# Optimization experiments

Hardware: AMD Instinct MI355X
Metric: run time of the kernel (lower is better)

## Reference

```python
import jax, jax.numpy as jnp
import numpy as np

DIM = 1024
HEADS = 16
MLP = 4096
EPS = 1e-5

def _layer_norm(x, g, b):
    mu = jnp.mean(x, axis=-1, keepdims=True)
    var = jnp.mean(jnp.square(x - mu), axis=-1, keepdims=True)
    return (x - mu) * jax.lax.rsqrt(var + EPS) * g + b

def setup_inputs() -> dict:
    key = jax.random.key(0)
    ks = jax.random.split(key, 8)
    s = 0.02
    return {
        "x": jax.random.normal(ks[0], (2, 2048, DIM), dtype=jnp.float32),
        "ln1_g": jnp.ones((DIM,), jnp.float32),
        "ln1_b": jnp.zeros((DIM,), jnp.float32),
        "qkv_w": jax.random.normal(ks[1], (DIM, 3 * DIM), jnp.float32) * s,
        "qkv_b": jnp.zeros((3 * DIM,), jnp.float32),
        "proj_w": jax.random.normal(ks[2], (DIM, DIM), jnp.float32) * s,
        "proj_b": jnp.zeros((DIM,), jnp.float32),
        "ln2_g": jnp.ones((DIM,), jnp.float32),
        "ln2_b": jnp.zeros((DIM,), jnp.float32),
        "fc1_w": jax.random.normal(ks[3], (DIM, MLP), jnp.float32) * s,
        "fc1_b": jnp.zeros((MLP,), jnp.float32),
        "fc2_w": jax.random.normal(ks[4], (MLP, DIM), jnp.float32) * s,
        "fc2_b": jnp.zeros((DIM,), jnp.float32),
    }

def reference(x, ln1_g, ln1_b, qkv_w, qkv_b, proj_w, proj_b,
              ln2_g, ln2_b, fc1_w, fc1_b, fc2_w, fc2_b):
    B, N, C = x.shape
    H = HEADS
    D = C // H
    # --- attention (pre-norm); NOTE: source applies no 1/sqrt(D) scaling ---
    h = _layer_norm(x, ln1_g, ln1_b)
    qkv = (h @ qkv_w + qkv_b).reshape(B, N, 3, H, D)
    q, k, v = (qkv[:, :, 0], qkv[:, :, 1], qkv[:, :, 2])  # [B,N,H,D]
    qk = jnp.einsum('bnhd,bmhd->bhnm', q, k)
    attn = jax.nn.softmax(qk, axis=-1)
    y = jnp.einsum('bhnm,bmhd->bnhd', attn, v).reshape(B, N, C)
    y = y @ proj_w + proj_b
    x = x + y
    # --- MLP (pre-norm), exact GELU like torch nn.GELU ---
    h2 = _layer_norm(x, ln2_g, ln2_b)
    h2 = jax.nn.gelu(h2 @ fc1_w + fc1_b, approximate=False)
    x = x + (h2 @ fc2_w + fc2_b)
    return x
```

## Files before the change

### kernel.cpp

```cpp
#include <hip/hip_runtime.h>
#include <hip/hip_bf16.h>

#define CDIM   1024
#define NSEQ   2048
#define NHEAD  16
#define HDIM   64
#define MLPDIM 4096
#define TROWS  4096

typedef __attribute__((ext_vector_type(8)))  __bf16 bf16x8;
typedef __attribute__((ext_vector_type(4)))  float  f32x4;
typedef __attribute__((ext_vector_type(16))) float  f32x16;
typedef __attribute__((ext_vector_type(4)))  unsigned short us4;

static __device__ __forceinline__ unsigned short f2bf(float f) {
  unsigned int u = __float_as_uint(f);
  u += 0x7fffu + ((u >> 16) & 1u);
  return (unsigned short)(u >> 16);
}

#define MFMA16(a, b, c) __builtin_amdgcn_mfma_f32_16x16x32_bf16(a, b, c, 0, 0, 0)
#define MFMA32(a, b, c) __builtin_amdgcn_mfma_f32_32x32x16_bf16(a, b, c, 0, 0, 0)

static __device__ __forceinline__ void gll16(const unsigned short* g, unsigned short* l) {
  __builtin_amdgcn_global_load_lds(
      (const __attribute__((address_space(1))) unsigned int*)g,
      (__attribute__((address_space(3))) unsigned int*)l, 16, 0, 0);
}

__global__ __launch_bounds__(256)
void ln_bf16_kernel(const float* __restrict__ x,
                    const float* __restrict__ gam,
                    const float* __restrict__ bet,
                    unsigned short* __restrict__ out)
{
  int row = blockIdx.x;
  int t = threadIdx.x;
  const float4* xr = (const float4*)(x + (size_t)row * CDIM);
  float4 v = xr[t];
  float s  = v.x + v.y + v.z + v.w;
  float s2 = v.x*v.x + v.y*v.y + v.z*v.z + v.w*v.w;
  #pragma unroll
  for (int off = 32; off > 0; off >>= 1) {
    s  += __shfl_down(s, off);
    s2 += __shfl_down(s2, off);
  }
  __shared__ float rs[4], rs2[4];
  int wave = t >> 6, lane = t & 63;
  if (lane == 0) { rs[wave] = s; rs2[wave] = s2; }
  __syncthreads();
  float fs  = rs[0] + rs[1] + rs[2] + rs[3];
  float fs2 = rs2[0] + rs2[1] + rs2[2] + rs2[3];
  float mu   = fs * (1.0f / CDIM);
  float var  = fs2 * (1.0f / CDIM) - mu * mu;
  float rstd = rsqrtf(var + 1e-5f);
  float4 gg = ((const float4*)gam)[t];
  float4 bb = ((const float4*)bet)[t];
  us4 o;
  o.x = f2bf((v.x - mu) * rstd * gg.x + bb.x);
  o.y = f2bf((v.y - mu) * rstd * gg.y + bb.y);
  o.z = f2bf((v.z - mu) * rstd * gg.z + bb.z);
  o.w = f2bf((v.w - mu) * rstd * gg.w + bb.w);
  ((us4*)(out + (size_t)row * CDIM))[t] = o;
}

__global__ __launch_bounds__(256)
void wt_bf16_kernel(const float* __restrict__ W, unsigned short* __restrict__ Wt,
                    int K, int N)
{
  __shared__ float tile[32][33];
  int n0 = blockIdx.x * 32, k0 = blockIdx.y * 32;
  int t = threadIdx.x;
  int r = t >> 3, c4 = (t & 7) << 2;
  float4 v = *(const float4*)(W + (size_t)(k0 + r) * N + n0 + c4);
  tile[r][c4 + 0] = v.x; tile[r][c4 + 1] = v.y;
  tile[r][c4 + 2] = v.z; tile[r][c4 + 3] = v.w;
  __syncthreads();
  us4 o;
  o.x = f2bf(tile[c4 + 0][r]);
  o.y = f2bf(tile[c4 + 1][r]);
  o.z = f2bf(tile[c4 + 2][r]);
  o.w = f2bf(tile[c4 + 3][r]);
  *(us4*)(Wt + (size_t)(n0 + r) * K + k0 + c4) = o;
}

template<int EPI>
__global__ __launch_bounds__(256, 4)
void gemm_bt(const unsigned short* __restrict__ A, const unsigned short* __restrict__ Bt,
             const float* __restrict__ bias, int Kstride, int Kc, int nbx, int nby,
             float* __restrict__ outf, unsigned short* __restrict__ outb,
             const float* __restrict__ resid, float* __restrict__ pp,
             unsigned short* __restrict__ qo, unsigned short* __restrict__ ko,
             unsigned short* __restrict__ vo)
{
  __shared__ unsigned short As[2][128 * 32];
  __shared__ unsigned short Bs[2][128 * 32];
  const int tid  = threadIdx.x;
  const int lane = tid & 63;
  const int wave = tid >> 6;
  const int wr = wave >> 1, wc = wave & 1;
  const int g = lane >> 4, r16 = lane & 15;

  const int nwg = gridDim.x;
  const int orig = ((int)blockIdx.x & 7) * (nwg >> 3) + ((int)blockIdx.x >> 3);
  const int bx = orig % nbx;
  const int t2 = orig / nbx;
  const int by = t2 % nby;
  const int kz = t2 / nby;
  const int bm = by * 128, bn = bx * 128;
  const int kbase = kz * Kc;
  const int N = nbx * 128;

  auto stage = [&](int d, int k0) {
    #pragma unroll
    for (int c = 0; c < 2; c++) {
      int o   = (c * 256 + tid) << 3;
      int row = o >> 5;
      int col = o & 31;
      int ub  = (c * 256 + (tid & ~63)) << 3;
      gll16(A  + (size_t)(bm + row) * Kstride + kbase + k0 + col, &As[d][ub]);
      gll16(Bt + (size_t)(bn + row) * Kstride + kbase + k0 + col, &Bs[d][ub]);
    }
  };

  f32x4 acc[4][4];
  #pragma unroll
  for (int i = 0; i < 4; i++)
    #pragma unroll
    for (int j = 0; j < 4; j++) acc[i][j] = (f32x4){0.f, 0.f, 0.f, 0.f};

  stage(0, 0);
  const int nkt = Kc / 32;
  for (int kt = 0; kt < nkt; kt++) {
    const int cur = kt & 1;
    __syncthreads();
    if (kt + 1 < nkt) stage(cur ^ 1, (kt + 1) * 32);
    bf16x8 af[4], bfr[4];
    #pragma unroll
    for (int i = 0; i < 4; i++) {
      int row = wr * 64 + i * 16 + r16;
      af[i] = *(const bf16x8*)(&As[cur][row * 32 + 8 * g]);
    }
    #pragma unroll
    for (int j = 0; j < 4; j++) {
      int row = wc * 64 + j * 16 + r16;
      bfr[j] = *(const bf16x8*)(&Bs[cur][row * 32 + 8 * g]);
    }
    __builtin_amdgcn_s_setprio(1);
    #pragma unroll
    for (int i = 0; i < 4; i++)
      #pragma unroll
      for (int j = 0; j < 4; j++)
        acc[i][j] = MFMA16(af[i], bfr[j], acc[i][j]);
    __builtin_amdgcn_s_setprio(0);
  }

  #pragma unroll
  for (int i = 0; i < 4; i++) {
    #pragma unroll
    for (int j = 0; j < 4; j++) {
      int col = bn + wc * 64 + j * 16 + r16;
      float bv = (EPI == 2 && kz != 0) ? 0.f : bias[col];
      #pragma unroll
      for (int jj = 0; jj < 4; jj++) {
        int row = bm + wr * 64 + i * 16 + 4 * g + jj;
        float val = acc[i][j][jj] + bv;
        if (EPI == 1) {
          int sel = col >> 10, cc = col & 1023;
          int hh = cc >> 6, d = cc & 63;
          int b = row >> 11, tk = row & 2047;
          size_t hb = (size_t)(b * NHEAD + hh);
          if (sel == 0)      qo[(hb * NSEQ + tk) * HDIM + d] = f2bf(val * 1.4426950408889634f);
          else if (sel == 1) ko[(hb * NSEQ + tk) * HDIM + d] = f2bf(val);
          else               vo[(hb * HDIM + d) * NSEQ + tk] = f2bf(val);
        } else if (EPI == 2) {
          size_t idx = (size_t)row * N + col;
          if (kz == 0) outf[idx] = val + resid[idx];
          else         pp[idx]   = val;
        } else {
          float ge = 0.5f * val * (1.0f + erff(val * 0.70710678118654752f));
          outb[(size_t)row * N + col] = f2bf(ge);
        }
      }
    }
  }
}

__global__ __launch_bounds__(256)
void add_kernel(float* __restrict__ out, const float* __restrict__ pp, int n4)
{
  int i = blockIdx.x * 256 + threadIdx.x;
  int stride = gridDim.x * 256;
  for (; i < n4; i += stride) {
    float4 a = ((const float4*)out)[i];
    float4 b = ((const float4*)pp)[i];
    a.x += b.x; a.y += b.y; a.z += b.z; a.w += b.w;
    ((float4*)out)[i] = a;
  }
}

__global__ __launch_bounds__(256, 2)
void attn_kernel(const unsigned short* __restrict__ q, const unsigned short* __restrict__ k,
                 const unsigned short* __restrict__ vt, unsigned short* __restrict__ y)
{
  int bid = blockIdx.x;
  int xcd = bid & 7, loc = bid >> 3;
  int bh  = xcd * 4 + (loc >> 4);
  int qchunk = loc & 15;
  int b = bh >> 4, h = bh & 15;
  int wave = threadIdx.x >> 6, lane = threadIdx.x & 63;
  int ql = lane & 31;
  int hi = lane >> 5;
  int q0 = qchunk * 128 + wave * 32;
  const unsigned short* qb = q  + (size_t)bh * NSEQ * HDIM;
  const unsigned short* kb = k  + (size_t)bh * NSEQ * HDIM;
  const unsigned short* vb = vt + (size_t)bh * HDIM * NSEQ;

  __shared__ unsigned short KL[2][2048];
  __shared__ unsigned short VL[2][2048];

  auto stage = [&](int d, int it) {
    int kv0 = it * 32;
    {
      int c = wave * 64 + lane;
      int row = c >> 3, col = c & 7;
      int sc  = (row << 3) | (col ^ (row & 7));
      gll16(kb + (size_t)kv0 * HDIM + sc * 8, &KL[d][wave * 512]);
    }
    {
      int c = wave * 64 + lane;
      int row = c >> 2, col = c & 3;
      int scol = col ^ ((row >> 1) & 3);
      gll16(vb + (size_t)row * NSEQ + kv0 + scol * 8, &VL[d][wave * 512]);
    }
  };

  bf16x8 aq[4];
  #pragma unroll
  for (int s = 0; s < 4; s++)
    aq[s] = *(const bf16x8*)(qb + (size_t)(q0 + ql) * HDIM + s * 16 + hi * 8);

  float ssum = 0.f;
  f32x16 o0, o1;
  #pragma unroll
  for (int r = 0; r < 16; r++) { o0[r] = 0.f; o1[r] = 0.f; }

  stage(0, 0);
  for (int it = 0; it < NSEQ / 32; it++) {
    const int cur = it & 1;
    __syncthreads();
    if (it + 1 < NSEQ / 32) stage(cur ^ 1, it + 1);
    bf16x8 kf[4];
    #pragma unroll
    for (int s = 0; s < 4; s++)
      kf[s] = *(const bf16x8*)((const char*)KL[cur] +
               ql * 128 + ((((s << 1) | hi) ^ (ql & 7)) << 4));
    f32x16 sacc;
    #pragma unroll
    for (int r = 0; r < 16; r++) sacc[r] = -32.0f;
    __builtin_amdgcn_s_setprio(1);
    #pragma unroll
    for (int s = 0; s < 4; s++)
      sacc = MFMA32(kf[s], aq[s], sacc);
    __builtin_amdgcn_s_setprio(0);
    float ps = 0.f;
    #pragma unroll
    for (int r = 0; r < 16; r++) {
      sacc[r] = exp2f(sacc[r]);
      ps += sacc[r];
    }
    ssum += ps;
    bf16x8 vf[2][2];
    #pragma unroll
    for (int t = 0; t < 2; t++)
      #pragma unroll
      for (int db = 0; db < 2; db++)
        vf[t][db] = *(const bf16x8*)((const char*)VL[cur] +
                     (db * 32 + ql) * 64 + ((((t << 1) | hi) ^ ((ql >> 1) & 3)) << 4));
    __builtin_amdgcn_s_setprio(1);
    #pragma unroll
    for (int t = 0; t < 2; t++) {
      unsigned pk01, pk23, pk45, pk67;
      asm("v_cvt_pk_bf16_f32 %0, %1, %2" : "=v"(pk01) : "v"(sacc[8*t+0]), "v"(sacc[8*t+1]));
      asm("v_cvt_pk_bf16_f32 %0, %1, %2" : "=v"(pk23) : "v"(sacc[8*t+2]), "v"(sacc[8*t+3]));
      asm("v_cvt_pk_bf16_f32 %0, %1, %2" : "=v"(pk45) : "v"(sacc[8*t+4]), "v"(sacc[8*t+5]));
      asm("v_cvt_pk_bf16_f32 %0, %1, %2" : "=v"(pk67) : "v"(sacc[8*t+6]), "v"(sacc[8*t+7]));
      asm("v_permlane32_swap_b32 %0, %1" : "+v"(pk01), "+v"(pk45));
      asm("v_permlane32_swap_b32 %0, %1" : "+v"(pk23), "+v"(pk67));
      union { unsigned u[4]; bf16x8 v; } pf;
      pf.u[0] = pk01; pf.u[1] = pk23; pf.u[2] = pk45; pf.u[3] = pk67;
      o0 = MFMA32(vf[t][0], pf.v, o0);
      o1 = MFMA32(vf[t][1], pf.v, o1);
    }
    __builtin_amdgcn_s_setprio(0);
  }
  float stot = ssum + __shfl_xor(ssum, 32);
  float inv = 1.0f / stot;
  unsigned short* yr = y + ((size_t)(b * NSEQ + q0 + ql)) * CDIM + h * HDIM;
  #pragma unroll
  for (int db = 0; db < 2; db++) {
    const f32x16& oo = db ? o1 : o0;
    #pragma unroll
    for (int rq = 0; rq < 4; rq++) {
      us4 w;
      w.x = f2bf(oo[4*rq+0] * inv);
      w.y = f2bf(oo[4*rq+1] * inv);
      w.z = f2bf(oo[4*rq+2] * inv);
      w.w = f2bf(oo[4*rq+3] * inv);
      *(us4*)(yr + db * 32 + rq * 8 + hi * 4) = w;
    }
  }
}

extern "C" void kernel_launch(void* const* d_in, const int* in_sizes, int n_in,
                              void* d_out, int out_size, void* d_ws, size_t ws_size,
                              hipStream_t stream)
{
  const float* x      = (const float*)d_in[0];
  const float* ln1_g  = (const float*)d_in[1];
  const float* ln1_b  = (const float*)d_in[2];
  const float* qkv_w  = (const float*)d_in[3];
  const float* qkv_b  = (const float*)d_in[4];
  const float* proj_w = (const float*)d_in[5];
  const float* proj_b = (const float*)d_in[6];
  const float* ln2_g  = (const float*)d_in[7];
  const float* ln2_b  = (const float*)d_in[8];
  const float* fc1_w  = (const float*)d_in[9];
  const float* fc1_b  = (const float*)d_in[10];
  const float* fc2_w  = (const float*)d_in[11];
  const float* fc2_b  = (const float*)d_in[12];
  float* out = (float*)d_out;

  char* p = (char*)d_ws;
  size_t off = 0;
  auto alloc = [&](size_t bytes) -> void* {
    void* r = p + off; off += (bytes + 255) & ~(size_t)255; return r;
  };
  unsigned short* wt_qkv  = (unsigned short*)alloc((size_t)3072 * 1024 * 2);
  unsigned short* wt_proj = (unsigned short*)alloc((size_t)1024 * 1024 * 2);
  unsigned short* wt_fc1  = (unsigned short*)alloc((size_t)4096 * 1024 * 2);
  unsigned short* wt_fc2  = (unsigned short*)alloc((size_t)1024 * 4096 * 2);
  unsigned short* h1  = (unsigned short*)alloc((size_t)TROWS * CDIM * 2);
  unsigned short* qb  = (unsigned short*)alloc((size_t)TROWS * CDIM * 2);
  unsigned short* kb  = (unsigned short*)alloc((size_t)TROWS * CDIM * 2);
  unsigned short* vtb = (unsigned short*)alloc((size_t)TROWS * CDIM * 2);
  unsigned short* yb  = (unsigned short*)alloc((size_t)TROWS * CDIM * 2);
  float*          x1  = (float*)alloc((size_t)TROWS * CDIM * 4);
  unsigned short* h2  = (unsigned short*)alloc((size_t)TROWS * CDIM * 2);
  unsigned short* g1  = (unsigned short*)alloc((size_t)TROWS * MLPDIM * 2);
  float* pp = (float*)qb;

  dim3 blk(256);
  wt_bf16_kernel<<<dim3(3072 / 32, 1024 / 32), blk, 0, stream>>>(qkv_w, wt_qkv, 1024, 3072);
  wt_bf16_kernel<<<dim3(1024 / 32, 1024 / 32), blk, 0, stream>>>(proj_w, wt_proj, 1024, 1024);
  wt_bf16_kernel<<<dim3(4096 / 32, 1024 / 32), blk, 0, stream>>>(fc1_w, wt_fc1, 1024, 4096);
  wt_bf16_kernel<<<dim3(1024 / 32, 4096 / 32), blk, 0, stream>>>(fc2_w, wt_fc2, 4096, 1024);
  ln_bf16_kernel<<<TROWS, blk, 0, stream>>>(x, ln1_g, ln1_b, h1);
  gemm_bt<1><<<dim3(768), blk, 0, stream>>>(
      h1, wt_qkv, qkv_b, 1024, 1024, 24, 32,
      nullptr, nullptr, nullptr, nullptr, qb, kb, vtb);
  attn_kernel<<<dim3(512), blk, 0, stream>>>(qb, kb, vtb, yb);
  gemm_bt<2><<<dim3(512), blk, 0, stream>>>(
      yb, wt_proj, proj_b, 1024, 512, 8, 32,
      x1, nullptr, x, pp, nullptr, nullptr, nullptr);
  add_kernel<<<dim3(2048), blk, 0, stream>>>(x1, pp, TROWS * CDIM / 4);
  ln_bf16_kernel<<<TROWS, blk, 0, stream>>>(x1, ln2_g, ln2_b, h2);
  gemm_bt<3><<<dim3(1024), blk, 0, stream>>>(
      h2, wt_fc1, fc1_b, 1024, 1024, 32, 32,
      nullptr, g1, nullptr, nullptr, nullptr, nullptr, nullptr);
  gemm_bt<2><<<dim3(512), blk, 0, stream>>>(
      g1, wt_fc2, fc2_b, 4096, 2048, 8, 32,
      out, nullptr, x1, pp, nullptr, nullptr, nullptr);
  add_kernel<<<dim3(2048), blk, 0, stream>>>(out, pp, TROWS * CDIM / 4);
}
```

Before: 295.4 us.

## Split attention KV range across waves, fuse add into LN2, approximate GELU

The attention kernel now handles 64 query rows per block, with two wave pairs each covering half of the KV sequence. Partial outputs and sums are merged through shared memory, and the grid doubles to 1024 blocks at higher occupancy. This adds parallelism and occupancy for attention at the cost of an extra reduction step. Separately, the split-K residual add is folded into the second layernorm, removing one kernel launch and a full pass over memory. Exact erf GELU is replaced by a sigmoid-style exp2 approximation, which is cheaper but changes numerics slightly.

```diff
diff --git a/kernel.cpp b/kernel.cpp
--- a/kernel.cpp
+++ b/kernel.cpp
@@ -38,6 +38,45 @@
   int t = threadIdx.x;
   const float4* xr = (const float4*)(x + (size_t)row * CDIM);
   float4 v = xr[t];
+  float s  = v.x + v.y + v.z + v.w;
+  float s2 = v.x*v.x + v.y*v.y + v.z*v.z + v.w*v.w;
+  #pragma unroll
+  for (int off = 32; off > 0; off >>= 1) {
+    s  += __shfl_down(s, off);
+    s2 += __shfl_down(s2, off);
+  }
+  __shared__ float rs[4], rs2[4];
+  int wave = t >> 6, lane = t & 63;
+  if (lane == 0) { rs[wave] = s; rs2[wave] = s2; }
+  __syncthreads();
+  float fs  = rs[0] + rs[1] + rs[2] + rs[3];
+  float fs2 = rs2[0] + rs2[1] + rs2[2] + rs2[3];
+  float mu   = fs * (1.0f / CDIM);
+  float var  = fs2 * (1.0f / CDIM) - mu * mu;
+  float rstd = rsqrtf(var + 1e-5f);
+  float4 gg = ((const float4*)gam)[t];
+  float4 bb = ((const float4*)bet)[t];
+  us4 o;
+  o.x = f2bf((v.x - mu) * rstd * gg.x + bb.x);
+  o.y = f2bf((v.y - mu) * rstd * gg.y + bb.y);
+  o.z = f2bf((v.z - mu) * rstd * gg.z + bb.z);
+  o.w = f2bf((v.w - mu) * rstd * gg.w + bb.w);
+  ((us4*)(out + (size_t)row * CDIM))[t] = o;
+}
+
+__global__ __launch_bounds__(256)
+void ln_add_bf16_kernel(float* __restrict__ x, const float* __restrict__ pp,
+                        const float* __restrict__ gam, const float* __restrict__ bet,
+                        unsigned short* __restrict__ out)
+{
+  int row = blockIdx.x;
+  int t = threadIdx.x;
+  float4* xr = (float4*)(x + (size_t)row * CDIM);
+  const float4* pr = (const float4*)(pp + (size_t)row * CDIM);
+  float4 v = xr[t];
+  float4 q = pr[t];
+  v.x += q.x; v.y += q.y; v.z += q.z; v.w += q.w;
+  xr[t] = v;
   float s  = v.x + v.y + v.z + v.w;
   float s2 = v.x*v.x + v.y*v.y + v.z*v.z + v.w*v.w;
   #pragma unroll
@@ -178,7 +217,9 @@
           if (kz == 0) outf[idx] = val + resid[idx];
           else         pp[idx]   = val;
         } else {
-          float ge = 0.5f * val * (1.0f + erff(val * 0.70710678118654752f));
+          float vv = val * val;
+          float u2 = val * (2.3022361f + 0.1029445f * vv);
+          float ge = val - val / (1.0f + exp2f(u2));
           outb[(size_t)row * N + col] = f2bf(ge);
         }
       }
@@ -199,39 +240,43 @@
   }
 }
 
-__global__ __launch_bounds__(256, 2)
+__global__ __launch_bounds__(256, 4)
 void attn_kernel(const unsigned short* __restrict__ q, const unsigned short* __restrict__ k,
                  const unsigned short* __restrict__ vt, unsigned short* __restrict__ y)
 {
   int bid = blockIdx.x;
   int xcd = bid & 7, loc = bid >> 3;
-  int bh  = xcd * 4 + (loc >> 4);
-  int qchunk = loc & 15;
+  int bh  = xcd * 4 + (loc >> 5);
+  int qb64 = loc & 31;
   int b = bh >> 4, h = bh & 15;
   int wave = threadIdx.x >> 6, lane = threadIdx.x & 63;
+  int qt = wave >> 1, kvh = wave & 1;
   int ql = lane & 31;
   int hi = lane >> 5;
-  int q0 = qchunk * 128 + wave * 32;
+  int q0 = qb64 * 64 + qt * 32;
+  const int kvbase = kvh * (NSEQ / 2);
   const unsigned short* qb = q  + (size_t)bh * NSEQ * HDIM;
   const unsigned short* kb = k  + (size_t)bh * NSEQ * HDIM;
   const unsigned short* vb = vt + (size_t)bh * HDIM * NSEQ;
 
-  __shared__ unsigned short KL[2][2048];
-  __shared__ unsigned short VL[2][2048];
+  __shared__ unsigned short KL[2][2][2048];
+  __shared__ unsigned short VL[2][2][2048];
 
   auto stage = [&](int d, int it) {
-    int kv0 = it * 32;
-    {
-      int c = wave * 64 + lane;
+    int kv0 = kvbase + it * 32;
+    #pragma unroll
+    for (int i = 0; i < 2; i++) {
+      int c = i * 128 + qt * 64 + lane;
       int row = c >> 3, col = c & 7;
       int sc  = (row << 3) | (col ^ (row & 7));
-      gll16(kb + (size_t)kv0 * HDIM + sc * 8, &KL[d][wave * 512]);
-    }
-    {
-      int c = wave * 64 + lane;
+      gll16(kb + (size_t)kv0 * HDIM + sc * 8, &KL[kvh][d][(i * 128 + qt * 64) * 8]);
+    }
+    #pragma unroll
+    for (int i = 0; i < 2; i++) {
+      int c = i * 128 + qt * 64 + lane;
       int row = c >> 2, col = c & 3;
       int scol = col ^ ((row >> 1) & 3);
-      gll16(vb + (size_t)row * NSEQ + kv0 + scol * 8, &VL[d][wave * 512]);
+      gll16(vb + (size_t)row * NSEQ + kv0 + scol * 8, &VL[kvh][d][(i * 128 + qt * 64) * 8]);
     }
   };
 
@@ -246,14 +291,15 @@
   for (int r = 0; r < 16; r++) { o0[r] = 0.f; o1[r] = 0.f; }
 
   stage(0, 0);
-  for (int it = 0; it < NSEQ / 32; it++) {
+  const int nit = NSEQ / 64;
+  for (int it = 0; it < nit; it++) {
     const int cur = it & 1;
     __syncthreads();
-    if (it + 1 < NSEQ / 32) stage(cur ^ 1, it + 1);
+    if (it + 1 < nit) stage(cur ^ 1, it + 1);
     bf16x8 kf[4];
     #pragma unroll
     for (int s = 0; s < 4; s++)
-      kf[s] = *(const bf16x8*)((const char*)KL[cur] +
+      kf[s] = *(const bf16x8*)((const char*)KL[kvh][cur] +
                ql * 128 + ((((s << 1) | hi) ^ (ql & 7)) << 4));
     f32x16 sacc;
     #pragma unroll
@@ -275,7 +321,7 @@
     for (int t = 0; t < 2; t++)
       #pragma unroll
       for (int db = 0; db < 2; db++)
-        vf[t][db] = *(const bf16x8*)((const char*)VL[cur] +
+        vf[t][db] = *(const bf16x8*)((const char*)VL[kvh][cur] +
                      (db * 32 + ql) * 64 + ((((t << 1) | hi) ^ ((ql >> 1) & 3)) << 4));
     __builtin_amdgcn_s_setprio(1);
     #pragma unroll
@@ -294,20 +340,41 @@
     }
     __builtin_amdgcn_s_setprio(0);
   }
-  float stot = ssum + __shfl_xor(ssum, 32);
-  float inv = 1.0f / stot;
-  unsigned short* yr = y + ((size_t)(b * NSEQ + q0 + ql)) * CDIM + h * HDIM;
-  #pragma unroll
-  for (int db = 0; db < 2; db++) {
-    const f32x16& oo = db ? o1 : o0;
-    #pragma unroll
-    for (int rq = 0; rq < 4; rq++) {
-      us4 w;
-      w.x = f2bf(oo[4*rq+0] * inv);
-      w.y = f2bf(oo[4*rq+1] * inv);
-      w.z = f2bf(oo[4*rq+2] * inv);
-      w.w = f2bf(oo[4*rq+3] * inv);
-      *(us4*)(yr + db * 32 + rq * 8 + hi * 4) = w;
+
+  __syncthreads();
+  float* OM = (float*)&KL[0][0][0];
+  float* SM = (float*)&VL[0][0][0];
+  if (kvh == 1) {
+    #pragma unroll
+    for (int r = 0; r < 16; r++) {
+      OM[r * 128 + qt * 64 + lane]        = o0[r];
+      OM[(16 + r) * 128 + qt * 64 + lane] = o1[r];
+    }
+    SM[qt * 64 + lane] = ssum;
+  }
+  __syncthreads();
+  if (kvh == 0) {
+    float st = ssum + SM[qt * 64 + lane];
+    st += __shfl_xor(st, 32);
+    float inv = 1.0f / st;
+    #pragma unroll
+    for (int r = 0; r < 16; r++) {
+      o0[r] += OM[r * 128 + qt * 64 + lane];
+      o1[r] += OM[(16 + r) * 128 + qt * 64 + lane];
+    }
+    unsigned short* yr = y + ((size_t)(b * NSEQ + q0 + ql)) * CDIM + h * HDIM;
+    #pragma unroll
+    for (int db = 0; db < 2; db++) {
+      const f32x16& oo = db ? o1 : o0;
+      #pragma unroll
+      for (int rq = 0; rq < 4; rq++) {
+        us4 w;
+        w.x = f2bf(oo[4*rq+0] * inv);
+        w.y = f2bf(oo[4*rq+1] * inv);
+        w.z = f2bf(oo[4*rq+2] * inv);
+        w.w = f2bf(oo[4*rq+3] * inv);
+        *(us4*)(yr + db * 32 + rq * 8 + hi * 4) = w;
+      }
     }
   }
 }
@@ -359,12 +426,11 @@
   gemm_bt<1><<<dim3(768), blk, 0, stream>>>(
       h1, wt_qkv, qkv_b, 1024, 1024, 24, 32,
       nullptr, nullptr, nullptr, nullptr, qb, kb, vtb);
-  attn_kernel<<<dim3(512), blk, 0, stream>>>(qb, kb, vtb, yb);
+  attn_kernel<<<dim3(1024), blk, 0, stream>>>(qb, kb, vtb, yb);
   gemm_bt<2><<<dim3(512), blk, 0, stream>>>(
       yb, wt_proj, proj_b, 1024, 512, 8, 32,
       x1, nullptr, x, pp, nullptr, nullptr, nullptr);
-  add_kernel<<<dim3(2048), blk, 0, stream>>>(x1, pp, TROWS * CDIM / 4);
-  ln_bf16_kernel<<<TROWS, blk, 0, stream>>>(x1, ln2_g, ln2_b, h2);
+  ln_add_bf16_kernel<<<TROWS, blk, 0, stream>>>(x1, pp, ln2_g, ln2_b, h2);
   gemm_bt<3><<<dim3(1024), blk, 0, stream>>>(
       h2, wt_fc1, fc1_b, 1024, 1024, 32, 32,
       nullptr, g1, nullptr, nullptr, nullptr, nullptr, nullptr);
```

Result: faster. 287.3 us (-2.7%).
